# Performance work log

Hardware: AMD Instinct MI355X
Metric: run time of the kernel (lower is better)

Reference implementation:

```python
import jax, jax.numpy as jnp
import numpy as np

BATCH = 1024
DIM = 1024      # input_size == hidden_size (required by h0 = z.repeat(...))
BAR = 32
EPS = 1e-5


def setup_inputs() -> dict:
    key = jax.random.key(0)
    ks = jax.random.split(key, 13)
    s_in = 1.0 / np.sqrt(DIM)
    return {
        "z": jax.random.normal(ks[0], (BATCH, DIM), dtype=jnp.float32),
        "bn_gamma": jnp.ones((DIM,), jnp.float32),
        "bn_beta": jnp.zeros((DIM,), jnp.float32),
        # PyTorch LSTM params, gate order (i, f, g, o), shape (4H, in)
        "W_ih0": jax.random.uniform(ks[1], (4 * DIM, DIM), jnp.float32, -s_in, s_in),
        "W_hh0": jax.random.uniform(ks[2], (4 * DIM, DIM), jnp.float32, -s_in, s_in),
        "b_ih0": jax.random.uniform(ks[3], (4 * DIM,), jnp.float32, -s_in, s_in),
        "b_hh0": jax.random.uniform(ks[4], (4 * DIM,), jnp.float32, -s_in, s_in),
        "W_ih1": jax.random.uniform(ks[5], (4 * DIM, DIM), jnp.float32, -s_in, s_in),
        "W_hh1": jax.random.uniform(ks[6], (4 * DIM, DIM), jnp.float32, -s_in, s_in),
        "b_ih1": jax.random.uniform(ks[7], (4 * DIM,), jnp.float32, -s_in, s_in),
        "b_hh1": jax.random.uniform(ks[8], (4 * DIM,), jnp.float32, -s_in, s_in),
        "W_lin": jax.random.uniform(ks[9], (DIM, DIM), jnp.float32, -s_in, s_in),
        "b_lin": jax.random.uniform(ks[10], (DIM,), jnp.float32, -s_in, s_in),
    }


def _lstm_cell(x_proj, h, c, W_hh, b_hh):
    # x_proj already contains x @ W_ih^T + b_ih
    gates = x_proj + h @ W_hh.T + b_hh          # (B, 4H)
    i, f, g, o = jnp.split(gates, 4, axis=-1)   # PyTorch gate order i,f,g,o
    c_new = jax.nn.sigmoid(f) * c + jax.nn.sigmoid(i) * jnp.tanh(g)
    h_new = jax.nn.sigmoid(o) * jnp.tanh(c_new)
    return h_new, c_new


def reference(z, bn_gamma, bn_beta, W_ih0, W_hh0, b_ih0, b_hh0,
              W_ih1, W_hh1, b_ih1, b_hh1, W_lin, b_lin):
    # BatchNorm1d in training mode (batch statistics, biased variance)
    mean = jnp.mean(z, axis=0)
    var = jnp.var(z, axis=0)
    zn = (z - mean) * jax.lax.rsqrt(var + EPS) * bn_gamma + bn_beta  # (B, D)

    # h0 = c0 = zn for both layers (init_hidden repeats z num_hidden times)
    # Layer-0 input is the constant zn every step -> precompute its projection
    x0_proj = zn @ W_ih0.T + b_ih0  # (B, 4H)

    def step(carry, _):
        h0, c0, h1, c1 = carry
        h0, c0 = _lstm_cell(x0_proj, h0, c0, W_hh0, b_hh0)
        x1_proj = h0 @ W_ih1.T + b_ih1
        h1, c1 = _lstm_cell(x1_proj, h1, c1, W_hh1, b_hh1)
        return (h0, c0, h1, c1), h1

    _, feats = jax.lax.scan(step, (zn, zn, zn, zn), None, length=BAR)
    feat = jnp.transpose(feats, (1, 0, 2))      # (B, bar, H)
    return feat @ W_lin.T + b_lin
```

## Files before the change

### kernel.cpp

```cpp
#include <hip/hip_runtime.h>

#define DEV __device__ __forceinline__

typedef unsigned short u16;
using bf16x8 = __attribute__((ext_vector_type(8))) __bf16;
using f32x4  = __attribute__((ext_vector_type(4))) float;

DEV u16 f2bf(float f){
  unsigned u = __float_as_uint(f);
  u += 0x7fffu + ((u >> 16) & 1u);
  return (u16)(u >> 16);
}
DEV float sigf(float x){ return 1.f / (1.f + __expf(-x)); }
DEV float tanh_(float x){ return 2.f / (1.f + __expf(-2.f*x)) - 1.f; }

DEV void async16(const u16* g, u16* l){
  __builtin_amdgcn_global_load_lds(
      (const __attribute__((address_space(1))) unsigned int*)g,
      (__attribute__((address_space(3))) unsigned int*)l, 16, 0, 0);
}

__global__ void bn_stats(const float* __restrict__ z, float* __restrict__ ps, float* __restrict__ pq){
  int bx = blockIdx.x; int rg = bx >> 2, cg = bx & 3;
  int c = cg*256 + threadIdx.x;
  float s = 0.f, q = 0.f;
  for (int r = rg*64; r < rg*64 + 64; ++r){ float v = z[r*1024 + c]; s += v; q += v*v; }
  ps[rg*1024 + c] = s; pq[rg*1024 + c] = q;
}

__global__ void bn_fin(const float* __restrict__ ps, const float* __restrict__ pq,
                       const float* __restrict__ gam, const float* __restrict__ bet,
                       float* __restrict__ sc, float* __restrict__ sh){
  int c = blockIdx.x*256 + threadIdx.x;
  float s = 0.f, q = 0.f;
  for (int rg = 0; rg < 16; ++rg){ s += ps[rg*1024 + c]; q += pq[rg*1024 + c]; }
  float mean = s * (1.f/1024.f);
  float var  = q * (1.f/1024.f) - mean*mean;
  float k = gam[c] * rsqrtf(var + 1e-5f);
  sc[c] = k; sh[c] = bet[c] - mean*k;
}

__global__ void bn_norm(const float* __restrict__ z, const float* __restrict__ sc, const float* __restrict__ sh,
                        u16* __restrict__ h0, u16* __restrict__ h1,
                        float* __restrict__ c0, float* __restrict__ c1){
  int bx = blockIdx.x; int rg = bx >> 2, cg = bx & 3;
  int c = cg*256 + threadIdx.x;
  float k = sc[c], b = sh[c];
  for (int r = rg*64; r < rg*64 + 64; ++r){
    float v = z[r*1024 + c]*k + b;
    u16 hv = f2bf(v);
    h0[r*1024 + c] = hv; h1[r*1024 + c] = hv;
    c0[r*1024 + c] = v;  c1[r*1024 + c] = v;
  }
}

__global__ void conv_w(const float* __restrict__ src, u16* __restrict__ dst,
                       int dstStride, int colOff, int permute){
  int c = blockIdx.x;
  int row = c;
  if (permute){ int gate = (c>>4)&3; int u = (c&15) | ((c>>6)<<4); row = (gate<<10) + u; }
  float4 v = ((const float4*)(src + (size_t)row*1024))[threadIdx.x];
  ushort4 o; o.x = f2bf(v.x); o.y = f2bf(v.y); o.z = f2bf(v.z); o.w = f2bf(v.w);
  ((ushort4*)(dst + (size_t)c*dstStride + colOff))[threadIdx.x] = o;
}

__global__ void bias_k(const float* __restrict__ bi0, const float* __restrict__ bh0,
                       const float* __restrict__ bi1, const float* __restrict__ bh1,
                       float* __restrict__ bx0, float* __restrict__ b1){
  int c = blockIdx.x*256 + threadIdx.x;
  int gate = (c>>4)&3; int u = (c&15) | ((c>>6)<<4); int r = (gate<<10) + u;
  bx0[c] = bi0[r] + bh0[r];
  b1[c]  = bi1[r] + bh1[r];
}

template<int MODE>
DEV void gemm_core(int bx, int by,
                   const u16* __restrict__ A0, const u16* __restrict__ A1, int KloA,
                   const u16* __restrict__ Bm, int K,
                   const float* __restrict__ add, float* __restrict__ cst,
                   u16* __restrict__ hout, u16* __restrict__ hout2,
                   float* __restrict__ outf,
                   u16* sA, u16* sB)
{
  const int t = threadIdx.x;
  const int lane = t & 63;
  const int w = t >> 6, wm = w >> 1, wn = w & 1;
  const int m0 = by*128, n0 = bx*128;

  f32x4 acc[4][4];
#pragma unroll
  for (int i = 0; i < 4; ++i)
#pragma unroll
    for (int j = 0; j < 4; ++j) acc[i][j] = (f32x4){0.f,0.f,0.f,0.f};

  const int srow = t >> 3;
  const int kswz = (((t & 7) ^ ((t >> 3) & 7)) << 3);
  const int nkt = K >> 6;

  auto stageM = [&](const u16* P, int ld, int r0, int k0, u16* dst){
#pragma unroll
    for (int p = 0; p < 4; ++p)
      async16(P + (size_t)(r0 + p*32 + srow)*ld + k0 + kswz,
              dst + p*2048 + t*8);
  };
  auto stage = [&](int kt, int b){
    const int k0 = kt << 6;
    const u16* aPart; int kk;
    if (k0 < KloA){ aPart = A0; kk = k0; } else { aPart = A1; kk = k0 - KloA; }
    stageM(aPart, 1024, m0, kk, sA + b*8192);
    stageM(Bm,    K,    n0, k0, sB + b*8192);
  };

  const int rsel = lane >> 4;
  const int rxor = lane & 7;

  stage(0, 0);
  asm volatile("s_waitcnt vmcnt(0)" ::: "memory");
  __builtin_amdgcn_sched_barrier(0);
  __builtin_amdgcn_s_barrier();
  __builtin_amdgcn_sched_barrier(0);

  for (int kt = 0; kt < nkt; ++kt){
    if (kt + 1 < nkt) stage(kt + 1, (kt + 1) & 1);
    const u16* pA = sA + (kt & 1)*8192;
    const u16* pB = sB + (kt & 1)*8192;
#pragma unroll
    for (int ksub = 0; ksub < 2; ++ksub){
      bf16x8 af[4], bfr[4];
#pragma unroll
      for (int i = 0; i < 4; ++i){
        int ra = wm*64 + i*16 + (lane & 15);
        int rb = wn*64 + i*16 + (lane & 15);
        int sl = ((ksub*4 + rsel) ^ rxor) << 3;
        af[i]  = *(const bf16x8*)&pA[ra*64 + sl];
        bfr[i] = *(const bf16x8*)&pB[rb*64 + sl];
      }
      __builtin_amdgcn_s_setprio(1);
#pragma unroll
      for (int i = 0; i < 4; ++i)
#pragma unroll
        for (int j = 0; j < 4; ++j)
          acc[i][j] = __builtin_amdgcn_mfma_f32_16x16x32_bf16(af[i], bfr[j], acc[i][j], 0, 0, 0);
      __builtin_amdgcn_s_setprio(0);
    }
    if (kt + 1 < nkt){
      asm volatile("s_waitcnt vmcnt(0)" ::: "memory");
      __builtin_amdgcn_sched_barrier(0);
      __builtin_amdgcn_s_barrier();
      __builtin_amdgcn_sched_barrier(0);
    }
  }

  const int s  = lane & 15;
  const int rq = (lane >> 4) * 4;

  if constexpr (MODE == 0 || MODE == 3){
    const int ldc = (MODE == 0) ? 4096 : 1024;
#pragma unroll
    for (int j = 0; j < 4; ++j){
      int col = n0 + wn*64 + j*16 + s;
      float bj = add[col];
#pragma unroll
      for (int i = 0; i < 4; ++i){
        int rowb = m0 + wm*64 + i*16 + rq;
#pragma unroll
        for (int r = 0; r < 4; ++r)
          outf[(size_t)(rowb + r)*ldc + col] = acc[i][j][r] + bj;
      }
    }
  } else {
    const int u = s + ((bx*2 + wn) << 4);
    int cidx[4]; float bj[4];
#pragma unroll
    for (int j = 0; j < 4; ++j){
      cidx[j] = n0 + wn*64 + j*16 + s;
      if (MODE == 2) bj[j] = add[cidx[j]];
    }
#pragma unroll
    for (int i = 0; i < 4; ++i){
      int rowb = m0 + wm*64 + i*16 + rq;
#pragma unroll
      for (int r = 0; r < 4; ++r){
        int row = rowb + r;
        float g0, g1, g2, g3;
        if (MODE == 1){
          const float* xp = add + (size_t)row*4096;
          g0 = acc[i][0][r] + xp[cidx[0]];
          g1 = acc[i][1][r] + xp[cidx[1]];
          g2 = acc[i][2][r] + xp[cidx[2]];
          g3 = acc[i][3][r] + xp[cidx[3]];
        } else {
          g0 = acc[i][0][r] + bj[0];
          g1 = acc[i][1][r] + bj[1];
          g2 = acc[i][2][r] + bj[2];
          g3 = acc[i][3][r] + bj[3];
        }
        float ig = sigf(g0), fg = sigf(g1), gg = tanh_(g2), og = sigf(g3);
        size_t si = (size_t)row*1024 + u;
        float cn = fg * cst[si] + ig * gg;
        cst[si] = cn;
        float hn = og * tanh_(cn);
        u16 hb = f2bf(hn);
        hout[si] = hb;
        if (MODE == 2) hout2[(size_t)row*32768 + u] = hb;
      }
    }
  }
}

template<int MODE, int SWZ>
__global__ __launch_bounds__(256)
void gemm_k(const u16* __restrict__ A0, const u16* __restrict__ Bm, int K,
            const float* __restrict__ add, float* __restrict__ outf)
{
  __shared__ __align__(16) u16 sA[2*8192];
  __shared__ __align__(16) u16 sB[2*8192];
  int bx = blockIdx.x, by = blockIdx.y;
  if constexpr (SWZ){
    int lin = by * (int)gridDim.x + bx;
    int xcd = lin & 7, idx = lin >> 3;
    by = xcd*32 + (idx >> 3);
    bx = idx & 7;
  }
  gemm_core<MODE>(bx, by, A0, nullptr, 1<<20, Bm, K, add,
                  nullptr, nullptr, nullptr, outf, sA, sB);
}

__global__ __launch_bounds__(256)
void fused_step(const u16* __restrict__ h0in, const u16* __restrict__ h1in,
                const u16* __restrict__ Whh0p, const u16* __restrict__ W1p,
                const float* __restrict__ X0p, const float* __restrict__ B1,
                float* __restrict__ C0, float* __restrict__ C1,
                u16* __restrict__ h0out, u16* __restrict__ h1out,
                u16* __restrict__ feats, int roles)
{
  __shared__ __align__(16) u16 sA[2*8192];
  __shared__ __align__(16) u16 sB[2*8192];
  int by = blockIdx.y, isL0;
  if (roles == 0){ isL0 = (by >= 8); by &= 7; }
  else isL0 = (roles == 1);
  if (isL0)
    gemm_core<1>(blockIdx.x, by, h0in, nullptr, 1<<20, Whh0p, 1024, X0p,
                 C0, h0out, nullptr, nullptr, sA, sB);
  else
    gemm_core<2>(blockIdx.x, by, h0in, h1in, 1024, W1p, 2048, B1,
                 C1, h1out, feats, nullptr, sA, sB);
}

extern "C" void kernel_launch(void* const* d_in, const int* in_sizes, int n_in,
                              void* d_out, int out_size, void* d_ws, size_t ws_size,
                              hipStream_t stream)
{
  (void)in_sizes; (void)n_in; (void)out_size; (void)ws_size;
  const float* z    = (const float*)d_in[0];
  const float* gam  = (const float*)d_in[1];
  const float* bet  = (const float*)d_in[2];
  const float* Wih0 = (const float*)d_in[3];
  const float* Whh0 = (const float*)d_in[4];
  const float* bih0 = (const float*)d_in[5];
  const float* bhh0 = (const float*)d_in[6];
  const float* Wih1 = (const float*)d_in[7];
  const float* Whh1 = (const float*)d_in[8];
  const float* bih1 = (const float*)d_in[9];
  const float* bhh1 = (const float*)d_in[10];
  const float* Wlin = (const float*)d_in[11];
  const float* blin = (const float*)d_in[12];
  float* out = (float*)d_out;

  char* p = (char*)d_ws;
  auto alloc = [&](size_t b) -> void* { void* r = (void*)p; p += (b + 255) & ~(size_t)255; return r; };
  u16*  Wih0p = (u16*)alloc((size_t)4096*1024*2);
  u16*  Whh0p = (u16*)alloc((size_t)4096*1024*2);
  u16*  W1p   = (u16*)alloc((size_t)4096*2048*2);
  u16*  Wlinp = (u16*)alloc((size_t)1024*1024*2);
  float* Bx0  = (float*)alloc(4096*4);
  float* B1   = (float*)alloc(4096*4);
  float* X0p  = (float*)alloc((size_t)1024*4096*4);
  u16*  H0a   = (u16*)alloc((size_t)1024*1024*2);
  u16*  H0b   = (u16*)alloc((size_t)1024*1024*2);
  u16*  H1a   = (u16*)alloc((size_t)1024*1024*2);
  u16*  H1b   = (u16*)alloc((size_t)1024*1024*2);
  float* C0   = (float*)alloc((size_t)1024*1024*4);
  float* C1   = (float*)alloc((size_t)1024*1024*4);
  u16*  Feats = (u16*)alloc((size_t)1024*32*1024*2);
  float* PS   = (float*)alloc(16*1024*4);
  float* PQ   = (float*)alloc(16*1024*4);
  float* Sc   = (float*)alloc(1024*4);
  float* Sh   = (float*)alloc(1024*4);

  bn_stats<<<64, 256, 0, stream>>>(z, PS, PQ);
  bn_fin<<<4, 256, 0, stream>>>(PS, PQ, gam, bet, Sc, Sh);
  bn_norm<<<64, 256, 0, stream>>>(z, Sc, Sh, H0a, H1a, C0, C1);
  conv_w<<<4096, 256, 0, stream>>>(Wih0, Wih0p, 1024, 0, 1);
  conv_w<<<4096, 256, 0, stream>>>(Whh0, Whh0p, 1024, 0, 1);
  conv_w<<<4096, 256, 0, stream>>>(Wih1, W1p, 2048, 0, 1);
  conv_w<<<4096, 256, 0, stream>>>(Whh1, W1p, 2048, 1024, 1);
  conv_w<<<1024, 256, 0, stream>>>(Wlin, Wlinp, 1024, 0, 0);
  bias_k<<<16, 256, 0, stream>>>(bih0, bhh0, bih1, bhh1, Bx0, B1);

  gemm_k<0,0><<<dim3(32,8), 256, 0, stream>>>(H0a, Wih0p, 1024, Bx0, X0p);

  u16* h0b[2] = {H0a, H0b};
  u16* h1b[2] = {H1a, H1b};

  fused_step<<<dim3(32,8), 256, 0, stream>>>(h0b[0], nullptr, Whh0p, W1p, X0p, B1,
                                             C0, C1, h0b[1], nullptr, nullptr, 1);
  for (int t = 0; t < 31; ++t){
    fused_step<<<dim3(32,16), 256, 0, stream>>>(
        h0b[(t+1)&1], h1b[t&1], Whh0p, W1p, X0p, B1,
        C0, C1, h0b[t&1], h1b[(t+1)&1], Feats + (size_t)t*1024, 0);
  }
  fused_step<<<dim3(32,8), 256, 0, stream>>>(h0b[0], h1b[1], Whh0p, W1p, X0p, B1,
                                             C0, C1, nullptr, h1b[0], Feats + (size_t)31*1024, 2);

  gemm_k<3,1><<<dim3(8,256), 256, 0, stream>>>(Feats, Wlinp, 1024, blin, out);
}
```

Baseline: 1.745 ms.

## Prepack weights in MFMA fragment order and load B directly to registers

Weights are now pre-packed into a fragment-ordered layout, so each wave loads its B operand straight from global memory into registers with contiguous 16-byte loads. This removes the B tile from LDS staging. The A tile moves to a three-buffer LDS ring with prefetch two tiles ahead and a partial vmcnt wait, overlapping loads with MFMA work. The costs are more global/L2 traffic for B, since each wave refetches its own B fragments instead of sharing them through LDS, and more register pressure from double-buffered B fragments.

```diff
diff --git a/kernel.cpp b/kernel.cpp
--- a/kernel.cpp
+++ b/kernel.cpp
@@ -54,14 +54,26 @@
   }
 }
 
-__global__ void conv_w(const float* __restrict__ src, u16* __restrict__ dst,
-                       int dstStride, int colOff, int permute){
-  int c = blockIdx.x;
-  int row = c;
-  if (permute){ int gate = (c>>4)&3; int u = (c&15) | ((c>>6)<<4); row = (gate<<10) + u; }
-  float4 v = ((const float4*)(src + (size_t)row*1024))[threadIdx.x];
-  ushort4 o; o.x = f2bf(v.x); o.y = f2bf(v.y); o.z = f2bf(v.z); o.w = f2bf(v.w);
-  ((ushort4*)(dst + (size_t)c*dstStride + colOff))[threadIdx.x] = o;
+__global__ void pack_w(const float* __restrict__ src0, const float* __restrict__ src1,
+                       int KloA, int K, int permute, u16* __restrict__ dst){
+  int c = blockIdx.x*4 + (threadIdx.x >> 6);
+  int lane = threadIdx.x & 63;
+  int j = c & 3, wn = (c>>2)&1, ksub = (c>>3)&1;
+  int rest = c >> 4;
+  int nkt = K >> 6;
+  int kt = rest % nkt, bx = rest / nkt;
+  int rn = bx*128 + wn*64 + j*16 + (lane & 15);
+  int row = rn;
+  if (permute){ int gate=(rn>>4)&3; int u=(rn&15)|((rn>>6)<<4); row=(gate<<10)+u; }
+  int k0 = kt*64 + ksub*32 + (lane>>4)*8;
+  const float* s; int kk;
+  if (k0 < KloA){ s = src0; kk = k0; } else { s = src1; kk = k0 - KloA; }
+  const float4* v = (const float4*)(s + (size_t)row*1024 + kk);
+  float4 a = v[0], b = v[1];
+  ushort4 o0; o0.x=f2bf(a.x); o0.y=f2bf(a.y); o0.z=f2bf(a.z); o0.w=f2bf(a.w);
+  ushort4 o1; o1.x=f2bf(b.x); o1.y=f2bf(b.y); o1.z=f2bf(b.z); o1.w=f2bf(b.w);
+  ushort4* d = (ushort4*)(dst + ((size_t)c<<9) + lane*8);
+  d[0]=o0; d[1]=o1;
 }
 
 __global__ void bias_k(const float* __restrict__ bi0, const float* __restrict__ bh0,
@@ -76,11 +88,11 @@
 template<int MODE>
 DEV void gemm_core(int bx, int by,
                    const u16* __restrict__ A0, const u16* __restrict__ A1, int KloA,
-                   const u16* __restrict__ Bm, int K,
+                   const u16* __restrict__ Bp, int K,
                    const float* __restrict__ add, float* __restrict__ cst,
                    u16* __restrict__ hout, u16* __restrict__ hout2,
                    float* __restrict__ outf,
-                   u16* sA, u16* sB)
+                   u16* sA)
 {
   const int t = threadIdx.x;
   const int lane = t & 63;
@@ -97,58 +109,78 @@
   const int kswz = (((t & 7) ^ ((t >> 3) & 7)) << 3);
   const int nkt = K >> 6;
 
-  auto stageM = [&](const u16* P, int ld, int r0, int k0, u16* dst){
-#pragma unroll
-    for (int p = 0; p < 4; ++p)
-      async16(P + (size_t)(r0 + p*32 + srow)*ld + k0 + kswz,
-              dst + p*2048 + t*8);
-  };
-  auto stage = [&](int kt, int b){
+  auto stageA = [&](int kt, int b){
     const int k0 = kt << 6;
     const u16* aPart; int kk;
     if (k0 < KloA){ aPart = A0; kk = k0; } else { aPart = A1; kk = k0 - KloA; }
-    stageM(aPart, 1024, m0, kk, sA + b*8192);
-    stageM(Bm,    K,    n0, k0, sB + b*8192);
+    u16* dst = sA + b*8192;
+#pragma unroll
+    for (int p = 0; p < 4; ++p)
+      async16(aPart + (size_t)(m0 + p*32 + srow)*1024 + kk + kswz,
+              dst + p*2048 + t*8);
+  };
+
+  const u16* BpL = Bp + lane*8;
+  auto loadB = [&](bf16x8* b, int kt, int ksub){
+    const u16* p = BpL + (((((size_t)bx*nkt + kt)*2 + ksub)*2 + wn) << 11);
+#pragma unroll
+    for (int j = 0; j < 4; ++j) b[j] = *(const bf16x8*)(p + (size_t)j*512);
   };
 
   const int rsel = lane >> 4;
   const int rxor = lane & 7;
 
-  stage(0, 0);
+  bf16x8 bP[4], bQ[4];
+  stageA(0, 0); stageA(1, 1);
+  loadB(bP, 0, 0);
   asm volatile("s_waitcnt vmcnt(0)" ::: "memory");
   __builtin_amdgcn_sched_barrier(0);
   __builtin_amdgcn_s_barrier();
   __builtin_amdgcn_sched_barrier(0);
 
   for (int kt = 0; kt < nkt; ++kt){
-    if (kt + 1 < nkt) stage(kt + 1, (kt + 1) & 1);
-    const u16* pA = sA + (kt & 1)*8192;
-    const u16* pB = sB + (kt & 1)*8192;
-#pragma unroll
-    for (int ksub = 0; ksub < 2; ++ksub){
-      bf16x8 af[4], bfr[4];
+    const u16* pA = sA + (kt % 3)*8192;
+    loadB(bQ, kt, 1);
+    {
+      bf16x8 af[4];
 #pragma unroll
       for (int i = 0; i < 4; ++i){
         int ra = wm*64 + i*16 + (lane & 15);
-        int rb = wn*64 + i*16 + (lane & 15);
-        int sl = ((ksub*4 + rsel) ^ rxor) << 3;
-        af[i]  = *(const bf16x8*)&pA[ra*64 + sl];
-        bfr[i] = *(const bf16x8*)&pB[rb*64 + sl];
+        int sl = ((0*4 + rsel) ^ rxor) << 3;
+        af[i] = *(const bf16x8*)&pA[ra*64 + sl];
       }
       __builtin_amdgcn_s_setprio(1);
 #pragma unroll
       for (int i = 0; i < 4; ++i)
 #pragma unroll
         for (int j = 0; j < 4; ++j)
-          acc[i][j] = __builtin_amdgcn_mfma_f32_16x16x32_bf16(af[i], bfr[j], acc[i][j], 0, 0, 0);
+          acc[i][j] = __builtin_amdgcn_mfma_f32_16x16x32_bf16(af[i], bP[j], acc[i][j], 0, 0, 0);
       __builtin_amdgcn_s_setprio(0);
     }
-    if (kt + 1 < nkt){
-      asm volatile("s_waitcnt vmcnt(0)" ::: "memory");
-      __builtin_amdgcn_sched_barrier(0);
-      __builtin_amdgcn_s_barrier();
-      __builtin_amdgcn_sched_barrier(0);
-    }
+    {
+      int ktn = (kt + 1 < nkt) ? kt + 1 : nkt - 1;
+      int kts = (kt + 2 < nkt) ? kt + 2 : nkt - 1;
+      loadB(bP, ktn, 0);
+      stageA(kts, (kt + 2) % 3);
+      bf16x8 af[4];
+#pragma unroll
+      for (int i = 0; i < 4; ++i){
+        int ra = wm*64 + i*16 + (lane & 15);
+        int sl = ((1*4 + rsel) ^ rxor) << 3;
+        af[i] = *(const bf16x8*)&pA[ra*64 + sl];
+      }
+      __builtin_amdgcn_s_setprio(1);
+#pragma unroll
+      for (int i = 0; i < 4; ++i)
+#pragma unroll
+        for (int j = 0; j < 4; ++j)
+          acc[i][j] = __builtin_amdgcn_mfma_f32_16x16x32_bf16(af[i], bQ[j], acc[i][j], 0, 0, 0);
+      __builtin_amdgcn_s_setprio(0);
+    }
+    asm volatile("s_waitcnt vmcnt(8)" ::: "memory");
+    __builtin_amdgcn_sched_barrier(0);
+    __builtin_amdgcn_s_barrier();
+    __builtin_amdgcn_sched_barrier(0);
   }
 
   const int s  = lane & 15;
@@ -210,11 +242,10 @@
 
 template<int MODE, int SWZ>
 __global__ __launch_bounds__(256)
-void gemm_k(const u16* __restrict__ A0, const u16* __restrict__ Bm, int K,
+void gemm_k(const u16* __restrict__ A0, const u16* __restrict__ Bp, int K,
             const float* __restrict__ add, float* __restrict__ outf)
 {
-  __shared__ __align__(16) u16 sA[2*8192];
-  __shared__ __align__(16) u16 sB[2*8192];
+  __shared__ __align__(16) u16 sA[3*8192];
   int bx = blockIdx.x, by = blockIdx.y;
   if constexpr (SWZ){
     int lin = by * (int)gridDim.x + bx;
@@ -222,8 +253,8 @@
     by = xcd*32 + (idx >> 3);
     bx = idx & 7;
   }
-  gemm_core<MODE>(bx, by, A0, nullptr, 1<<20, Bm, K, add,
-                  nullptr, nullptr, nullptr, outf, sA, sB);
+  gemm_core<MODE>(bx, by, A0, nullptr, 1<<20, Bp, K, add,
+                  nullptr, nullptr, nullptr, outf, sA);
 }
 
 __global__ __launch_bounds__(256)
@@ -234,17 +265,16 @@
                 u16* __restrict__ h0out, u16* __restrict__ h1out,
                 u16* __restrict__ feats, int roles)
 {
-  __shared__ __align__(16) u16 sA[2*8192];
-  __shared__ __align__(16) u16 sB[2*8192];
+  __shared__ __align__(16) u16 sA[3*8192];
   int by = blockIdx.y, isL0;
   if (roles == 0){ isL0 = (by >= 8); by &= 7; }
   else isL0 = (roles == 1);
   if (isL0)
     gemm_core<1>(blockIdx.x, by, h0in, nullptr, 1<<20, Whh0p, 1024, X0p,
-                 C0, h0out, nullptr, nullptr, sA, sB);
+                 C0, h0out, nullptr, nullptr, sA);
   else
     gemm_core<2>(blockIdx.x, by, h0in, h1in, 1024, W1p, 2048, B1,
-                 C1, h1out, feats, nullptr, sA, sB);
+                 C1, h1out, feats, nullptr, sA);
 }
 
 extern "C" void kernel_launch(void* const* d_in, const int* in_sizes, int n_in,
@@ -291,11 +321,10 @@
   bn_stats<<<64, 256, 0, stream>>>(z, PS, PQ);
   bn_fin<<<4, 256, 0, stream>>>(PS, PQ, gam, bet, Sc, Sh);
   bn_norm<<<64, 256, 0, stream>>>(z, Sc, Sh, H0a, H1a, C0, C1);
-  conv_w<<<4096, 256, 0, stream>>>(Wih0, Wih0p, 1024, 0, 1);
-  conv_w<<<4096, 256, 0, stream>>>(Whh0, Whh0p, 1024, 0, 1);
-  conv_w<<<4096, 256, 0, stream>>>(Wih1, W1p, 2048, 0, 1);
-  conv_w<<<4096, 256, 0, stream>>>(Whh1, W1p, 2048, 1024, 1);
-  conv_w<<<1024, 256, 0, stream>>>(Wlin, Wlinp, 1024, 0, 0);
+  pack_w<<<2048, 256, 0, stream>>>(Wih0, Wih0, 1<<20, 1024, 1, Wih0p);
+  pack_w<<<2048, 256, 0, stream>>>(Whh0, Whh0, 1<<20, 1024, 1, Whh0p);
+  pack_w<<<4096, 256, 0, stream>>>(Wih1, Whh1, 1024, 2048, 1, W1p);
+  pack_w<<< 512, 256, 0, stream>>>(Wlin, Wlin, 1<<20, 1024, 0, Wlinp);
   bias_k<<<16, 256, 0, stream>>>(bih0, bhh0, bih1, bhh1, Bx0, B1);
 
   gemm_k<0,0><<<dim3(32,8), 256, 0, stream>>>(H0a, Wih0p, 1024, Bx0, X0p);
```

Result: faster. 1.482 ms (-15.1%).
